# Kernel tuning notes

Hardware: AMD Instinct MI355X
Metric: run time of the kernel (lower is better)

Reference implementation:

```python
import jax, jax.numpy as jnp
import numpy as np

D_MODEL = 512
NUM_HEADS = 8
D_K = D_MODEL // NUM_HEADS
LN_EPS = 1e-5


def setup_inputs() -> dict:
    key = jax.random.key(0)
    ks = jax.random.split(key, 11)
    d = D_MODEL
    s = 1.0 / np.sqrt(d)
    return {
        "x": jax.random.normal(ks[0], (4, 2048, d), dtype=jnp.float32),
        "Wq": jax.random.uniform(ks[1], (d, d), jnp.float32, -s, s),
        "bq": jax.random.uniform(ks[2], (d,), jnp.float32, -s, s),
        "Wk": jax.random.uniform(ks[3], (d, d), jnp.float32, -s, s),
        "bk": jax.random.uniform(ks[4], (d,), jnp.float32, -s, s),
        "Wv": jax.random.uniform(ks[5], (d, d), jnp.float32, -s, s),
        "bv": jax.random.uniform(ks[6], (d,), jnp.float32, -s, s),
        "Wo": jax.random.uniform(ks[7], (d, d), jnp.float32, -s, s),
        "bo": jax.random.uniform(ks[8], (d,), jnp.float32, -s, s),
        "gamma": jnp.ones((d,), jnp.float32),
        "beta": jnp.zeros((d,), jnp.float32),
    }


def reference(x, Wq, bq, Wk, bk, Wv, bv, Wo, bo, gamma, beta):
    # x: (B, S, D). Dropout is identity (eval mode).
    B, S, D = x.shape
    H, dk = NUM_HEADS, D_K
    # Linear layers use torch convention: y = x @ W.T + b
    q = (x @ Wq.T + bq).reshape(B, S, H, dk).transpose(0, 2, 1, 3)  # (B,H,S,dk)
    k = (x @ Wk.T + bk).reshape(B, S, H, dk).transpose(0, 2, 1, 3)
    v = (x @ Wv.T + bv).reshape(B, S, H, dk).transpose(0, 2, 1, 3)
    scores = jnp.einsum("bhqd,bhkd->bhqk", q, k) / jnp.sqrt(jnp.float32(dk))
    attn = jax.nn.softmax(scores, axis=-1)
    ctx = jnp.einsum("bhqk,bhkd->bhqd", attn, v)  # (B,H,S,dk)
    ctx = ctx.transpose(0, 2, 1, 3).reshape(B, S, D)
    out = ctx @ Wo.T + bo
    # residual + LayerNorm
    y = x + out
    mu = jnp.mean(y, axis=-1, keepdims=True)
    var = jnp.mean(jnp.square(y - mu), axis=-1, keepdims=True)
    return (y - mu) / jnp.sqrt(var + LN_EPS) * gamma + beta
```

## Files before the change

kernel.cpp:

```cpp
#include <hip/hip_runtime.h>
#include <math.h>

#define D 512
#define NH 8
#define DK 64
#define S 2048
#define BATCH 4
#define N_TOK (BATCH * S)

#define QSCALE 0.18033688f

typedef __bf16 bf16x8 __attribute__((ext_vector_type(8)));
typedef __bf16 bf16x4 __attribute__((ext_vector_type(4)));
typedef float f32x4 __attribute__((ext_vector_type(4)));

#define AS1 __attribute__((address_space(1)))
#define AS3 __attribute__((address_space(3)))

#define OFF_XB   0
#define OFF_WB   8388608
#define OFF_Q    10485760
#define OFF_K    18874368
#define OFF_VT   27262976
#define OFF_CTX  35651584
#define OFF_Y    10485760
#define OFF_FLAG 44040192

static __device__ __forceinline__ bf16x8 ldg8(const __bf16* p) {
    return *(const bf16x8*)p;
}
static __device__ __forceinline__ f32x4 mfma16(bf16x8 a, bf16x8 b, f32x4 c) {
    return __builtin_amdgcn_mfma_f32_16x16x32_bf16(a, b, c, 0, 0, 0);
}
static __device__ __forceinline__ float ldf(const void* p, size_t i, int isf) {
    return isf ? ((const float*)p)[i] : (float)(((const __bf16*)p)[i]);
}
static __device__ __forceinline__ float fexp2(float x) {
#if __has_builtin(__builtin_amdgcn_exp2f)
    return __builtin_amdgcn_exp2f(x);
#else
    return exp2f(x);
#endif
}
static __device__ __forceinline__ unsigned pack_trunc(float e0, float e1) {
    return (__builtin_bit_cast(unsigned, e0) >> 16)
         | (__builtin_bit_cast(unsigned, e1) & 0xFFFF0000u);
}
static __device__ __forceinline__ void gload_lds16(const void* g, void* l) {
    __builtin_amdgcn_global_load_lds((const AS1 char*)g, (AS3 char*)l, 16, 0, 0);
}

__global__ __launch_bounds__(256)
void cvt_kernel(const void* __restrict__ x,  const void* __restrict__ Wq,
                const void* __restrict__ Wk, const void* __restrict__ Wv,
                const void* __restrict__ Wo, __bf16* __restrict__ xb,
                __bf16* __restrict__ Wb, int* __restrict__ flag)
{
    const bf16x8 probe = ldg8((const __bf16*)x + (threadIdx.x & 63) * 8);
    int bad = 0;
#pragma unroll
    for (int j = 0; j < 8; ++j) bad |= !(fabsf((float)probe[j]) <= 64.0f);
    const int isf = __any(bad) ? 1 : 0;
    if (blockIdx.x == 0 && threadIdx.x == 0) *flag = isf;

    const size_t i0 = ((size_t)blockIdx.x * 256 + threadIdx.x) * 8;
    const void* src;
    __bf16* dst;
    size_t off;
    if (i0 < 4194304) {
        src = x; off = i0; dst = xb + i0;
    } else {
        const size_t wrel = i0 - 4194304;
        const size_t w = wrel >> 18;
        src = (w == 0) ? Wq : (w == 1) ? Wk : (w == 2) ? Wv : Wo;
        off = wrel & 262143;
        dst = Wb + wrel;
    }
    bf16x8 r;
    if (isf) {
        const float* f = (const float*)src + off;
#pragma unroll
        for (int j = 0; j < 8; ++j) r[j] = (__bf16)f[j];
    } else {
        r = *(const bf16x8*)((const __bf16*)src + off);
    }
    *(bf16x8*)dst = r;
}

__global__ __launch_bounds__(256)
void qkv_kernel(const __bf16* __restrict__ xb, const __bf16* __restrict__ Wb,
                const void* __restrict__ bq, const void* __restrict__ bk,
                const void* __restrict__ bv, const int* __restrict__ flag,
                __bf16* __restrict__ Q, __bf16* __restrict__ K,
                __bf16* __restrict__ Vt)
{
    __shared__ __align__(16) char smem[32768];

    const int isf = *flag;
    const int tid = threadIdx.x;
    const int w = tid >> 6, l = tid & 63;
    const int lane16 = l & 15, quad = l >> 4;
    const int wm = w >> 1, wn = w & 1;
    const int m0 = blockIdx.x * 128;
    const int by = blockIdx.y;
    const int n0 = by * 128;

    const int cwl = w * 64 + l;
    const int g0 = (cwl & 3) ^ ((cwl >> 3) & 3);
    const __bf16* aS0 = xb + (size_t)(m0 + (cwl >> 2)) * D + g0 * 8;
    const __bf16* aS1 = aS0 + (size_t)64 * D;
    const __bf16* bS0 = Wb + (size_t)(n0 + (cwl >> 2)) * D + g0 * 8;
    const __bf16* bS1 = bS0 + (size_t)64 * D;

    const int sw = (quad ^ ((lane16 >> 1) & 3)) * 16;
    const int aoff = (wm * 64 + lane16) * 64 + sw;
    const int boff = 8192 + (wn * 64 + lane16) * 64 + sw;

    f32x4 acc[4][4];
#pragma unroll
    for (int i = 0; i < 4; ++i)
#pragma unroll
        for (int j = 0; j < 4; ++j) acc[i][j] = (f32x4){0,0,0,0};

    gload_lds16(aS0, smem + w * 1024);
    gload_lds16(aS1, smem + 4096 + w * 1024);
    gload_lds16(bS0, smem + 8192 + w * 1024);
    gload_lds16(bS1, smem + 12288 + w * 1024);

    for (int kt = 0; kt < D / 32; ++kt) {
        __syncthreads();

        const char* bufp = smem + (kt & 1) * 16384;
        if (kt + 1 < D / 32) {
            char* nb = smem + ((kt + 1) & 1) * 16384;
            gload_lds16(aS0 + (kt + 1) * 32, nb + w * 1024);
            gload_lds16(aS1 + (kt + 1) * 32, nb + 4096 + w * 1024);
            gload_lds16(bS0 + (kt + 1) * 32, nb + 8192 + w * 1024);
            gload_lds16(bS1 + (kt + 1) * 32, nb + 12288 + w * 1024);
        }

        bf16x8 af[4], bf[4];
#pragma unroll
        for (int i = 0; i < 4; ++i) af[i] = *(const bf16x8*)(bufp + aoff + i * 1024);
#pragma unroll
        for (int j = 0; j < 4; ++j) bf[j] = *(const bf16x8*)(bufp + boff + j * 1024);
#pragma unroll
        for (int i = 0; i < 4; ++i)
#pragma unroll
            for (int j = 0; j < 4; ++j)
                acc[i][j] = mfma16(af[i], bf[j], acc[i][j]);
    }

    const int which = by >> 2;
    const int h = (by * 2 + wn) & 7;
    const float qs = (which == 0) ? QSCALE : 1.0f;
    const void* bias = (which == 0) ? bq : (which == 1) ? bk : bv;
    float bvv[4];
#pragma unroll
    for (int j = 0; j < 4; ++j)
        bvv[j] = ldf(bias, ((by & 3) * 128 + wn * 64 + 16 * j + lane16) & 511, isf);

    const int bb = m0 >> 11;
    const int ssb = (m0 & (S - 1)) + wm * 64;

    if (which < 2) {
        __bf16* out = ((which == 0) ? Q : K) + ((size_t)(bb * NH + h) * S) * DK;
#pragma unroll
        for (int i = 0; i < 4; ++i)
#pragma unroll
            for (int r = 0; r < 4; ++r) {
                const int ss = ssb + i * 16 + quad * 4 + r;
#pragma unroll
                for (int j = 0; j < 4; ++j)
                    out[(size_t)ss * DK + 16 * j + lane16] =
                        (__bf16)((acc[i][j][r] + bvv[j]) * qs);
            }
    } else {
#pragma unroll
        for (int i = 0; i < 4; ++i)
#pragma unroll
            for (int j = 0; j < 4; ++j) {
                const int dkc = 16 * j + lane16;
                __bf16* vp = Vt + ((size_t)(bb * NH + h) * DK + dkc) * S
                                + ssb + i * 16 + quad * 4;
                bf16x4 pkt;
#pragma unroll
                for (int r = 0; r < 4; ++r) pkt[r] = (__bf16)(acc[i][j][r] + bvv[j]);
                *(bf16x4*)vp = pkt;
            }
    }
}

__global__ __launch_bounds__(512, 4)
void attn_kernel(const __bf16* __restrict__ Q, const __bf16* __restrict__ K,
                 const __bf16* __restrict__ Vt, __bf16* __restrict__ ctx)
{
    __shared__ __align__(16) char smem[49152];

    const int tid = threadIdx.x;
    const int w = tid >> 6, l = tid & 63;
    const int lane16 = l & 15, quad = l >> 4;

    const int lin = blockIdx.x;
    const int xcd = lin & 7;
    const int t = lin >> 3;
    const int bh = xcd * 4 + (t >> 4);
    const int qt = t & 15;
    const int b = bh >> 3, h = bh & 7;
    const size_t bhS = (size_t)bh * S;

    const int cwl = w * 64 + l;
    const int row = cwl >> 3;
    const int g = (cwl & 7) ^ (row & 7);
    const char* kS = (const char*)(K + (bhS + row) * DK) + g * 16;
    const char* vS = (const char*)(Vt + ((size_t)bh * DK + row) * S) + g * 16;

    const int qbase = qt * 128 + w * 16;
    bf16x8 qa0, qa1;
    {
        const __bf16* Qp = Q + (bhS + qbase + lane16) * DK + quad * 8;
        qa0 = ldg8(Qp);
        qa1 = ldg8(Qp + 32);
    }

    bf16x8 aones;
#pragma unroll
    for (int j = 0; j < 8; ++j) aones[j] = (__bf16)1.0f;

    const int x7 = lane16 & 7;
    char* pw = smem + 32768 + w * 2048;
    const int pwoff = lane16 * 128 + ((quad & 1) * 8);
    const int proff = lane16 * 128;

    f32x4 o[4], lacc;
    lacc = (f32x4){0,0,0,0};
#pragma unroll
    for (int tt = 0; tt < 4; ++tt) o[tt] = (f32x4){0,0,0,0};

    gload_lds16(kS, smem + w * 1024);
    gload_lds16(vS, smem + 8192 + w * 1024);

    for (int kc = 0; kc < S / 64; ++kc) {
        __syncthreads();

        const int buf = kc & 1;
        const char* kb = smem + buf * 16384;
        const char* vb = kb + 8192;

        if (kc + 1 < S / 64) {
            char* kb2 = smem + (buf ^ 1) * 16384;
            gload_lds16(kS + (size_t)(kc + 1) * 8192, kb2 + w * 1024);
            gload_lds16(vS + (size_t)(kc + 1) * 128, kb2 + 8192 + w * 1024);
        }

        bf16x8 kfA[4], kfB[4];
#pragma unroll
        for (int tt = 0; tt < 4; ++tt) {
            const int base = (tt * 16 + lane16) * 128;
            kfA[tt] = *(const bf16x8*)(kb + base + ((quad ^ x7) * 16));
            kfB[tt] = *(const bf16x8*)(kb + base + (((quad + 4) ^ x7) * 16));
        }

        {
            f32x4 st[4];
#pragma unroll
            for (int tt = 0; tt < 4; ++tt) {
                f32x4 z = {0,0,0,0};
                z = mfma16(kfA[tt], qa0, z);
                st[tt] = mfma16(kfB[tt], qa1, z);
            }
#pragma unroll
            for (int tt = 0; tt < 4; ++tt) {
                uint2 pkt;
                pkt.x = pack_trunc(fexp2(st[tt][0]), fexp2(st[tt][1]));
                pkt.y = pack_trunc(fexp2(st[tt][2]), fexp2(st[tt][3]));
                *(uint2*)(pw + pwoff
                          + (((tt * 2 + (quad >> 1)) ^ x7) * 16)) = pkt;
            }
        }

        bf16x8 vA[4], vB[4];
#pragma unroll
        for (int tt = 0; tt < 4; ++tt) {
            const int base = (tt * 16 + lane16) * 128;
            vA[tt] = *(const bf16x8*)(vb + base + ((quad ^ x7) * 16));
            vB[tt] = *(const bf16x8*)(vb + base + (((quad + 4) ^ x7) * 16));
        }
        {
            const bf16x8 bp0 = *(const bf16x8*)(pw + proff
                                                + (((0 + quad) ^ x7) * 16));
            const bf16x8 bp1 = *(const bf16x8*)(pw + proff
                                                + (((4 + quad) ^ x7) * 16));
            lacc = mfma16(aones, bp0, lacc);
            lacc = mfma16(aones, bp1, lacc);
#pragma unroll
            for (int tt = 0; tt < 4; ++tt) {
                o[tt] = mfma16(vA[tt], bp0, o[tt]);
                o[tt] = mfma16(vB[tt], bp1, o[tt]);
            }
        }
    }

    {
        const float inv = 1.0f / lacc[0];
        __bf16* cp = ctx + ((size_t)(b * S + qbase + lane16)) * D + h * DK;
#pragma unroll
        for (int tt = 0; tt < 4; ++tt) {
            bf16x4 pkt;
#pragma unroll
            for (int r = 0; r < 4; ++r) pkt[r] = (__bf16)(o[tt][r] * inv);
            *(bf16x4*)(cp + tt * 16 + quad * 4) = pkt;
        }
    }
}

__global__ __launch_bounds__(256)
void proj_kernel(const __bf16* __restrict__ ctx, const __bf16* __restrict__ Wb,
                 const void* __restrict__ bo, const __bf16* __restrict__ xb,
                 const int* __restrict__ flag, __bf16* __restrict__ y)
{
    __shared__ __align__(16) char smem[24576];

    const int isf = *flag;
    const int tid = threadIdx.x;
    const int w = tid >> 6, l = tid & 63;
    const int lane16 = l & 15, quad = l >> 4;
    const int wm = w >> 1, wn = w & 1;
    const int m0 = blockIdx.x * 64;
    const int n0 = blockIdx.y * 128;

    const __bf16* Wo = Wb + (size_t)3 * 262144;
    const int cwl = w * 64 + l;
    const int g0 = (cwl & 3) ^ ((cwl >> 3) & 3);
    const __bf16* aS = ctx + (size_t)(m0 + (cwl >> 2)) * D + g0 * 8;
    const __bf16* bS0 = Wo + (size_t)(n0 + (cwl >> 2)) * D + g0 * 8;
    const __bf16* bS1 = bS0 + (size_t)64 * D;

    const int sw = (quad ^ ((lane16 >> 1) & 3)) * 16;
    const int aoff = (wm * 32 + lane16) * 64 + sw;
    const int boff = 4096 + (wn * 64 + lane16) * 64 + sw;

    f32x4 acc[2][4];
#pragma unroll
    for (int i = 0; i < 2; ++i)
#pragma unroll
        for (int j = 0; j < 4; ++j) acc[i][j] = (f32x4){0,0,0,0};

    gload_lds16(aS, smem + w * 1024);
    gload_lds16(bS0, smem + 4096 + w * 1024);
    gload_lds16(bS1, smem + 8192 + w * 1024);

    for (int kt = 0; kt < D / 32; ++kt) {
        __syncthreads();

        const char* bufp = smem + (kt & 1) * 12288;
        if (kt + 1 < D / 32) {
            char* nb = smem + ((kt + 1) & 1) * 12288;
            gload_lds16(aS + (kt + 1) * 32, nb + w * 1024);
            gload_lds16(bS0 + (kt + 1) * 32, nb + 4096 + w * 1024);
            gload_lds16(bS1 + (kt + 1) * 32, nb + 8192 + w * 1024);
        }

        bf16x8 af[2], bf[4];
#pragma unroll
        for (int i = 0; i < 2; ++i) af[i] = *(const bf16x8*)(bufp + aoff + i * 1024);
#pragma unroll
        for (int j = 0; j < 4; ++j) bf[j] = *(const bf16x8*)(bufp + boff + j * 1024);
#pragma unroll
        for (int i = 0; i < 2; ++i)
#pragma unroll
            for (int j = 0; j < 4; ++j)
                acc[i][j] = mfma16(af[i], bf[j], acc[i][j]);
    }

    float bvv[4];
#pragma unroll
    for (int j = 0; j < 4; ++j)
        bvv[j] = ldf(bo, n0 + wn * 64 + 16 * j + lane16, isf);

#pragma unroll
    for (int i = 0; i < 2; ++i)
#pragma unroll
        for (int r = 0; r < 4; ++r) {
            const int tok = m0 + wm * 32 + i * 16 + quad * 4 + r;
#pragma unroll
            for (int j = 0; j < 4; ++j) {
                const size_t idx = (size_t)tok * D + n0 + wn * 64 + 16 * j + lane16;
                y[idx] = (__bf16)(acc[i][j][r] + bvv[j] + (float)xb[idx]);
            }
        }
}

__global__ __launch_bounds__(256)
void ln_kernel(const __bf16* __restrict__ y, const void* __restrict__ gamma,
               const void* __restrict__ beta, const int* __restrict__ flag,
               void* __restrict__ out)
{
    const int isf = *flag;
    const int l = threadIdx.x & 63;
    const int tok = blockIdx.x * 4 + (threadIdx.x >> 6);
    const bf16x8 vv = ldg8(y + (size_t)tok * D + l * 8);

    float v[8];
    float sum = 0.f, sq = 0.f;
#pragma unroll
    for (int j = 0; j < 8; ++j) {
        v[j] = (float)vv[j];
        sum += v[j];
        sq  += v[j] * v[j];
    }
#pragma unroll
    for (int msk = 1; msk < 64; msk <<= 1) {
        sum += __shfl_xor(sum, msk);
        sq  += __shfl_xor(sq,  msk);
    }
    const float mean = sum * (1.0f / D);
    const float var  = sq * (1.0f / D) - mean * mean;
    const float rstd = rsqrtf(var + 1e-5f);

    const size_t base = (size_t)tok * D + l * 8;
#pragma unroll
    for (int j = 0; j < 8; ++j) {
        const float g  = ldf(gamma, l * 8 + j, isf);
        const float be = ldf(beta,  l * 8 + j, isf);
        const float r  = ((v[j] - mean) * rstd) * g + be;
        if (isf) ((float*)out)[base + j] = r;
        else     ((__bf16*)out)[base + j] = (__bf16)r;
    }
}

extern "C" void kernel_launch(void* const* d_in, const int* in_sizes, int n_in,
                              void* d_out, int out_size, void* d_ws,
                              size_t ws_size, hipStream_t stream)
{
    const void* x     = d_in[0];
    const void* Wq    = d_in[1];
    const void* bq    = d_in[2];
    const void* Wk    = d_in[3];
    const void* bk    = d_in[4];
    const void* Wv    = d_in[5];
    const void* bv    = d_in[6];
    const void* Wo    = d_in[7];
    const void* bo    = d_in[8];
    const void* gamma = d_in[9];
    const void* beta  = d_in[10];

    char* ws = (char*)d_ws;
    __bf16* xb  = (__bf16*)(ws + OFF_XB);
    __bf16* Wb  = (__bf16*)(ws + OFF_WB);
    __bf16* Qb  = (__bf16*)(ws + OFF_Q);
    __bf16* Kb  = (__bf16*)(ws + OFF_K);
    __bf16* Vtb = (__bf16*)(ws + OFF_VT);
    __bf16* ctx = (__bf16*)(ws + OFF_CTX);
    __bf16* y   = (__bf16*)(ws + OFF_Y);
    int*    flag = (int*)(ws + OFF_FLAG);

    cvt_kernel<<<5242880 / (256 * 8), 256, 0, stream>>>(
        x, Wq, Wk, Wv, Wo, xb, Wb, flag);
    qkv_kernel<<<dim3(N_TOK / 128, 12), 256, 0, stream>>>(
        xb, Wb, bq, bk, bv, flag, Qb, Kb, Vtb);
    attn_kernel<<<dim3(512), 512, 0, stream>>>(Qb, Kb, Vtb, ctx);
    proj_kernel<<<dim3(N_TOK / 64, 4), 256, 0, stream>>>(
        ctx, Wb, bo, xb, flag, y);
    ln_kernel<<<dim3(N_TOK / 4), 256, 0, stream>>>(y, gamma, beta, flag, d_out);
}
```

Measured before the change: 183.1 us.

## Keep softmax probabilities in registers by permuting V^T key layout

The exp'd score tile is now packed directly into the MFMA B-operand registers instead of being written to and re-read from a per-wave LDS scratch area. To make the register layout match the P·V contraction order, the QKV kernel writes V^T with a permuted key ordering within each 64-key block. This removes the LDS round trip for P and shrinks shared memory from 48KB to 32KB, which could allow more blocks per CU. The key permutation must match exactly between producer and consumer, or the results will be wrong.

```diff
diff --git a/kernel.cpp b/kernel.cpp
--- a/kernel.cpp
+++ b/kernel.cpp
@@ -13,6 +13,7 @@
 typedef __bf16 bf16x8 __attribute__((ext_vector_type(8)));
 typedef __bf16 bf16x4 __attribute__((ext_vector_type(4)));
 typedef float f32x4 __attribute__((ext_vector_type(4)));
+typedef unsigned int u32x4 __attribute__((ext_vector_type(4)));
 
 #define AS1 __attribute__((address_space(1)))
 #define AS3 __attribute__((address_space(3)))
@@ -182,7 +183,7 @@
             for (int j = 0; j < 4; ++j) {
                 const int dkc = 16 * j + lane16;
                 __bf16* vp = Vt + ((size_t)(bb * NH + h) * DK + dkc) * S
-                                + ssb + i * 16 + quad * 4;
+                                + ssb + (quad + 4 * (i >> 1)) * 8 + 4 * (i & 1);
                 bf16x4 pkt;
 #pragma unroll
                 for (int r = 0; r < 4; ++r) pkt[r] = (__bf16)(acc[i][j][r] + bvv[j]);
@@ -195,7 +196,7 @@
 void attn_kernel(const __bf16* __restrict__ Q, const __bf16* __restrict__ K,
                  const __bf16* __restrict__ Vt, __bf16* __restrict__ ctx)
 {
-    __shared__ __align__(16) char smem[49152];
+    __shared__ __align__(16) char smem[32768];
 
     const int tid = threadIdx.x;
     const int w = tid >> 6, l = tid & 63;
@@ -228,9 +229,6 @@
     for (int j = 0; j < 8; ++j) aones[j] = (__bf16)1.0f;
 
     const int x7 = lane16 & 7;
-    char* pw = smem + 32768 + w * 2048;
-    const int pwoff = lane16 * 128 + ((quad & 1) * 8);
-    const int proff = lane16 * 128;
 
     f32x4 o[4], lacc;
     lacc = (f32x4){0,0,0,0};
@@ -248,9 +246,9 @@
         const char* vb = kb + 8192;
 
         if (kc + 1 < S / 64) {
-            char* kb2 = smem + (buf ^ 1) * 16384;
-            gload_lds16(kS + (size_t)(kc + 1) * 8192, kb2 + w * 1024);
-            gload_lds16(vS + (size_t)(kc + 1) * 128, kb2 + 8192 + w * 1024);
+            char* nb = smem + (buf ^ 1) * 16384;
+            gload_lds16(kS + (size_t)(kc + 1) * 8192, nb + w * 1024);
+            gload_lds16(vS + (size_t)(kc + 1) * 128, nb + 8192 + w * 1024);
         }
 
         bf16x8 kfA[4], kfB[4];
@@ -261,23 +259,25 @@
             kfB[tt] = *(const bf16x8*)(kb + base + (((quad + 4) ^ x7) * 16));
         }
 
-        {
-            f32x4 st[4];
-#pragma unroll
-            for (int tt = 0; tt < 4; ++tt) {
-                f32x4 z = {0,0,0,0};
-                z = mfma16(kfA[tt], qa0, z);
-                st[tt] = mfma16(kfB[tt], qa1, z);
-            }
-#pragma unroll
-            for (int tt = 0; tt < 4; ++tt) {
-                uint2 pkt;
-                pkt.x = pack_trunc(fexp2(st[tt][0]), fexp2(st[tt][1]));
-                pkt.y = pack_trunc(fexp2(st[tt][2]), fexp2(st[tt][3]));
-                *(uint2*)(pw + pwoff
-                          + (((tt * 2 + (quad >> 1)) ^ x7) * 16)) = pkt;
-            }
-        }
+        f32x4 st[4];
+#pragma unroll
+        for (int tt = 0; tt < 4; ++tt) {
+            f32x4 z = {0,0,0,0};
+            z = mfma16(kfA[tt], qa0, z);
+            st[tt] = mfma16(kfB[tt], qa1, z);
+        }
+
+        u32x4 u0, u1;
+        u0[0] = pack_trunc(fexp2(st[0][0]), fexp2(st[0][1]));
+        u0[1] = pack_trunc(fexp2(st[0][2]), fexp2(st[0][3]));
+        u0[2] = pack_trunc(fexp2(st[1][0]), fexp2(st[1][1]));
+        u0[3] = pack_trunc(fexp2(st[1][2]), fexp2(st[1][3]));
+        u1[0] = pack_trunc(fexp2(st[2][0]), fexp2(st[2][1]));
+        u1[1] = pack_trunc(fexp2(st[2][2]), fexp2(st[2][3]));
+        u1[2] = pack_trunc(fexp2(st[3][0]), fexp2(st[3][1]));
+        u1[3] = pack_trunc(fexp2(st[3][2]), fexp2(st[3][3]));
+        const bf16x8 bp0 = __builtin_bit_cast(bf16x8, u0);
+        const bf16x8 bp1 = __builtin_bit_cast(bf16x8, u1);
 
         bf16x8 vA[4], vB[4];
 #pragma unroll
@@ -286,18 +286,13 @@
             vA[tt] = *(const bf16x8*)(vb + base + ((quad ^ x7) * 16));
             vB[tt] = *(const bf16x8*)(vb + base + (((quad + 4) ^ x7) * 16));
         }
-        {
-            const bf16x8 bp0 = *(const bf16x8*)(pw + proff
-                                                + (((0 + quad) ^ x7) * 16));
-            const bf16x8 bp1 = *(const bf16x8*)(pw + proff
-                                                + (((4 + quad) ^ x7) * 16));
-            lacc = mfma16(aones, bp0, lacc);
-            lacc = mfma16(aones, bp1, lacc);
-#pragma unroll
-            for (int tt = 0; tt < 4; ++tt) {
-                o[tt] = mfma16(vA[tt], bp0, o[tt]);
-                o[tt] = mfma16(vB[tt], bp1, o[tt]);
-            }
+
+        lacc = mfma16(aones, bp0, lacc);
+        lacc = mfma16(aones, bp1, lacc);
+#pragma unroll
+        for (int tt = 0; tt < 4; ++tt) {
+            o[tt] = mfma16(vA[tt], bp0, o[tt]);
+            o[tt] = mfma16(vB[tt], bp1, o[tt]);
         }
     }
 
```

New measurement: 178.7 us. 2.4% less time.
